# Optimization experiments

Measured on AMD Instinct MI355X. Metric: run time of the kernel, lower is better.

The kernel has to match this reference:

```python
import jax, jax.numpy as jnp
import numpy as np

N_NODES = 50000


def setup_inputs() -> dict:
    key = jax.random.key(0)
    ks = jax.random.split(key, 6)
    d_in, d_out = 256, 256
    n_edges = 1_600_000
    x = jax.random.normal(ks[0], (N_NODES, d_in), dtype=jnp.float32)
    edge_index = jax.random.randint(ks[1], (2, n_edges), 0, N_NODES, dtype=jnp.int64)
    edge_attr = jax.random.normal(ks[2], (n_edges, 16), dtype=jnp.float32)  # unused by forward
    W1 = jax.random.normal(ks[3], (d_in, d_out), dtype=jnp.float32) * (1.0 / np.sqrt(d_in))
    b1 = jnp.zeros((d_out,), dtype=jnp.float32)
    W2 = jax.random.normal(ks[4], (d_out, d_out), dtype=jnp.float32) * (1.0 / np.sqrt(d_out))
    b2 = jnp.zeros((d_out,), dtype=jnp.float32)
    eps = jnp.zeros((1,), dtype=jnp.float32)  # train_eps=True, init 0
    return {"x": x, "edge_index": edge_index, "edge_attr": edge_attr,
            "W1": W1, "b1": b1, "W2": W2, "b2": b2, "eps": eps}


def reference(x, edge_index, edge_attr, W1, b1, W2, b2, eps):
    src, dst = edge_index[0], edge_index[1]
    # sum aggregation: agg[i] = sum_{(j->i) in E} x[j]
    agg = jax.ops.segment_sum(x[src], dst, num_segments=N_NODES)  # [N, d_in]
    h = (1.0 + eps[0]) * x + agg
    # MLP: Linear -> ReLU -> (dropout=0) -> Linear
    h = jax.nn.relu(h @ W1 + b1)
    out = h @ W2 + b2
    return out
```

## Files before the change

### kernel.cpp

```cpp
#include <hip/hip_runtime.h>
#include <stdint.h>

#define NODES 50000
#define D 256
#define MP 50048
#define NBUCK 196
#define CAP 10240
#define EPB 4096
#define HS_LD 264
#define CAST_BLOCKS 12500

typedef short bf16x8 __attribute__((ext_vector_type(8)));
typedef float f32x4 __attribute__((ext_vector_type(4)));

__device__ inline unsigned short f2b(float f) {
    unsigned int u = __float_as_uint(f);
    unsigned int r = (u + 0x7fffu + ((u >> 16) & 1u)) >> 16;
    return (unsigned short)r;
}

__device__ inline bool ei_is64(const int* ei) {
    return (ei[1] | ei[3] | ei[5] | ei[7]) == 0;
}
__device__ inline int ei_get(const int* __restrict__ ei, long long pos, bool is64) {
    return is64 ? ei[2 * pos] : ei[(int)pos];
}

__global__ __launch_bounds__(256) void prep_kernel(const float* __restrict__ x,
                                                   unsigned short* __restrict__ xb,
                                                   int* __restrict__ bcnt,
                                                   const float* __restrict__ W1,
                                                   const float* __restrict__ W2,
                                                   unsigned short* __restrict__ P1,
                                                   unsigned short* __restrict__ P2,
                                                   int* __restrict__ offs, int E) {
    int blk = blockIdx.x;
    if (blk < CAST_BLOCKS) {
        if (blk == 0 && threadIdx.x < NBUCK) bcnt[threadIdx.x] = 0;
        if (blk == 0 && threadIdx.x == 0) offs[NODES] = E;
        int t = blk * 256 + threadIdx.x;
        float4 v = ((const float4*)x)[t];
        unsigned int lo = (unsigned int)f2b(v.x) | ((unsigned int)f2b(v.y) << 16);
        unsigned int hi = (unsigned int)f2b(v.z) | ((unsigned int)f2b(v.w) << 16);
        ((uint2*)xb)[t] = make_uint2(lo, hi);
    } else {
        int t = (blk - CAST_BLOCKS) * 256 + threadIdx.x;
        const float* W = (t < 8192) ? W1 : W2;
        unsigned short* P = (t < 8192) ? P1 : P2;
        int u = t & 8191;
        int lane = u & 63, nt = (u >> 6) & 15, s = u >> 10;
        int q = lane >> 4, n = nt * 16 + (lane & 15);
        int kbase = s * 32 + q * 8;
#pragma unroll
        for (int j = 0; j < 8; j++) P[u * 8 + j] = f2b(W[(kbase + j) * D + n]);
    }
}

__global__ __launch_bounds__(256) void partA_kernel(const int* __restrict__ ei, int E,
                                                    int* __restrict__ bcnt,
                                                    unsigned int* __restrict__ ebufT) {
    __shared__ int cnt[256];
    __shared__ int gbase[256];
    __shared__ int lcur[256];
    bool is64 = ei_is64(ei);
    int tid = threadIdx.x;
    cnt[tid] = 0;
    lcur[tid] = 0;
    __syncthreads();
    long long pairBase = ((long long)blockIdx.x * EPB) >> 1;
    unsigned int w[16];
    int bk[16];
#pragma unroll
    for (int r = 0; r < 8; r++) {
        long long pp = pairBase + (long long)r * 256 + tid;
        long long e0 = pp * 2;
        int s0 = 0, s1 = 0, d0 = 0, d1 = 0;
        bool v1 = (e0 + 1 < E), v0 = (e0 < E);
        if (v1) {
            if (is64) {
                uint4 sv = *(const uint4*)(ei + 4 * pp);
                uint4 dv = *(const uint4*)(ei + (size_t)2 * E + 4 * pp);
                s0 = (int)sv.x; s1 = (int)sv.z; d0 = (int)dv.x; d1 = (int)dv.z;
            } else {
                uint2 sv = *(const uint2*)(ei + 2 * pp);
                uint2 dv = *(const uint2*)(ei + (size_t)E + 2 * pp);
                s0 = (int)sv.x; s1 = (int)sv.y; d0 = (int)dv.x; d1 = (int)dv.y;
            }
        } else if (v0) {
            s0 = ei_get(ei, e0, is64);
            d0 = ei_get(ei, (long long)E + e0, is64);
        }
        bk[2 * r] = v0 ? (d0 >> 8) : -1;
        bk[2 * r + 1] = v1 ? (d1 >> 8) : -1;
        w[2 * r] = ((unsigned int)(d0 & 255) << 16) | (unsigned int)s0;
        w[2 * r + 1] = ((unsigned int)(d1 & 255) << 16) | (unsigned int)s1;
        if (v0) atomicAdd(&cnt[bk[2 * r]], 1);
        if (v1) atomicAdd(&cnt[bk[2 * r + 1]], 1);
    }
    __syncthreads();
    if (tid < NBUCK && cnt[tid] > 0) gbase[tid] = atomicAdd(&bcnt[tid], cnt[tid]);
    __syncthreads();
#pragma unroll
    for (int r = 0; r < 16; r++) {
        if (bk[r] >= 0) {
            int p = atomicAdd(&lcur[bk[r]], 1);
            ebufT[(size_t)bk[r] * CAP + gbase[bk[r]] + p] = w[r];
        }
    }
}

__global__ __launch_bounds__(1024) void partB_kernel(const int* __restrict__ bcnt,
                                                     const unsigned int* __restrict__ ebufT,
                                                     int* __restrict__ offs,
                                                     int* __restrict__ ebuf) {
    __shared__ int sb[256];
    __shared__ int ncnt[256];
    __shared__ int ncur[256];
    int b = blockIdx.x, tid = threadIdx.x;
    if (tid < 256) {
        sb[tid] = (tid < NBUCK) ? bcnt[tid] : 0;
        ncnt[tid] = 0;
    }
    __syncthreads();
    for (int off = 1; off < 256; off <<= 1) {
        int xv = 0;
        if (tid < 256 && tid >= off) xv = sb[tid - off];
        __syncthreads();
        if (tid < 256) sb[tid] += xv;
        __syncthreads();
    }
    int n = bcnt[b];
    int base = sb[b] - n;
    const unsigned int* reg = ebufT + (size_t)b * CAP;
    for (int i = tid; i < n; i += 1024) atomicAdd(&ncnt[reg[i] >> 16], 1);
    __syncthreads();
    int v = 0;
    if (tid < 256) {
        v = ncnt[tid];
        ncur[tid] = v;
    }
    __syncthreads();
    for (int off = 1; off < 256; off <<= 1) {
        int xv = 0;
        if (tid < 256 && tid >= off) xv = ncur[tid - off];
        __syncthreads();
        if (tid < 256) ncur[tid] += xv;
        __syncthreads();
    }
    if (tid < 256) {
        int excl = ncur[tid] - v;
        int node = b * 256 + tid;
        if (node < NODES) offs[node] = base + excl;
        ncur[tid] = excl;
    }
    __syncthreads();
    for (int i = tid; i < n; i += 1024) {
        unsigned int w = reg[i];
        int p = atomicAdd(&ncur[w >> 16], 1);
        ebuf[base + p] = (int)(w & 0xffffu);
    }
}

__device__ inline void upk_add(uint4 w, float* a) {
    a[0] += __uint_as_float(w.x << 16);
    a[1] += __uint_as_float(w.x & 0xffff0000u);
    a[2] += __uint_as_float(w.y << 16);
    a[3] += __uint_as_float(w.y & 0xffff0000u);
    a[4] += __uint_as_float(w.z << 16);
    a[5] += __uint_as_float(w.z & 0xffff0000u);
    a[6] += __uint_as_float(w.w << 16);
    a[7] += __uint_as_float(w.w & 0xffff0000u);
}

__global__ __launch_bounds__(256) void agg_kernel(const unsigned short* __restrict__ xb,
                                                  const int* __restrict__ offs,
                                                  const int* __restrict__ ebuf,
                                                  const float* __restrict__ eps,
                                                  unsigned short* __restrict__ h0, int colOff) {
    int wv = (blockIdx.x * 256 + threadIdx.x) >> 6;
    int lane = threadIdx.x & 63;
    if (wv >= NODES) return;
    int g = lane >> 4, l16 = lane & 15;
    const unsigned short* colBase = xb + colOff + l16 * 8;
    float aA[8] = {0, 0, 0, 0, 0, 0, 0, 0};
    float aB[8] = {0, 0, 0, 0, 0, 0, 0, 0};
    int beg = offs[wv], end = offs[wv + 1];
    int j = beg;
    for (; j + 8 <= end; j += 8) {
        int i0 = ebuf[j + g];
        int i1 = ebuf[j + 4 + g];
        uint4 w0 = *(const uint4*)(colBase + (size_t)i0 * D);
        uint4 w1 = *(const uint4*)(colBase + (size_t)i1 * D);
        upk_add(w0, aA);
        upk_add(w1, aB);
    }
    for (; j + 4 <= end; j += 4) {
        int i0 = ebuf[j + g];
        uint4 w0 = *(const uint4*)(colBase + (size_t)i0 * D);
        upk_add(w0, aA);
    }
    if (j + g < end) {
        int i0 = ebuf[j + g];
        uint4 w0 = *(const uint4*)(colBase + (size_t)i0 * D);
        upk_add(w0, aA);
    }
    float a[8];
#pragma unroll
    for (int i = 0; i < 8; i++) {
        a[i] = aA[i] + aB[i];
        a[i] += __shfl_xor(a[i], 16);
        a[i] += __shfl_xor(a[i], 32);
    }
    if (g == 0) {
        float scale = 1.0f + eps[0];
        uint4 v = *(const uint4*)(xb + (size_t)wv * D + colOff + l16 * 8);
        a[0] += scale * __uint_as_float(v.x << 16);
        a[1] += scale * __uint_as_float(v.x & 0xffff0000u);
        a[2] += scale * __uint_as_float(v.y << 16);
        a[3] += scale * __uint_as_float(v.y & 0xffff0000u);
        a[4] += scale * __uint_as_float(v.z << 16);
        a[5] += scale * __uint_as_float(v.z & 0xffff0000u);
        a[6] += scale * __uint_as_float(v.w << 16);
        a[7] += scale * __uint_as_float(v.w & 0xffff0000u);
        uint4 o;
        o.x = (unsigned int)f2b(a[0]) | ((unsigned int)f2b(a[1]) << 16);
        o.y = (unsigned int)f2b(a[2]) | ((unsigned int)f2b(a[3]) << 16);
        o.z = (unsigned int)f2b(a[4]) | ((unsigned int)f2b(a[5]) << 16);
        o.w = (unsigned int)f2b(a[6]) | ((unsigned int)f2b(a[7]) << 16);
        ((uint4*)(h0 + (size_t)wv * D + colOff))[l16] = o;
    }
}

__global__ __launch_bounds__(256) void gemm_fused_kernel(const unsigned short* __restrict__ A,
                                                         const unsigned short* __restrict__ P1,
                                                         const float* __restrict__ b1,
                                                         const unsigned short* __restrict__ P2,
                                                         const float* __restrict__ b2,
                                                         float* __restrict__ out, int Mvalid) {
    __shared__ unsigned short hs[64 * HS_LD];
    int wv = threadIdx.x >> 6;
    int lane = threadIdx.x & 63;
    int quad = lane >> 4, l16 = lane & 15;
    int mBase = blockIdx.x * 64;
    const bf16x8* B1v = (const bf16x8*)P1;
    const bf16x8* B2v = (const bf16x8*)P2;

    {
        f32x4 acc[4][4] = {};
#pragma unroll
        for (int ks = 0; ks < 8; ks++) {
            bf16x8 af[4], bf[4];
#pragma unroll
            for (int mi = 0; mi < 4; mi++) {
                int row = mBase + mi * 16 + l16;
                af[mi] = *(const bf16x8*)(A + (size_t)row * D + ks * 32 + quad * 8);
            }
#pragma unroll
            for (int ni = 0; ni < 4; ni++) bf[ni] = B1v[(ks * 16 + wv * 4 + ni) * 64 + lane];
#pragma unroll
            for (int mi = 0; mi < 4; mi++)
#pragma unroll
                for (int ni = 0; ni < 4; ni++)
                    acc[mi][ni] = __builtin_amdgcn_mfma_f32_16x16x32_bf16(af[mi], bf[ni],
                                                                          acc[mi][ni], 0, 0, 0);
        }
#pragma unroll
        for (int mi = 0; mi < 4; mi++)
#pragma unroll
            for (int ni = 0; ni < 4; ni++) {
                int col = wv * 64 + ni * 16 + l16;
                float bs = b1[col];
#pragma unroll
                for (int r = 0; r < 4; r++) {
                    int rl = mi * 16 + quad * 4 + r;
                    hs[rl * HS_LD + col] = f2b(fmaxf(acc[mi][ni][r] + bs, 0.0f));
                }
            }
    }
    __syncthreads();

    f32x4 acc[4][4] = {};
#pragma unroll
    for (int ks = 0; ks < 8; ks++) {
        bf16x8 af[4], bf[4];
#pragma unroll
        for (int mi = 0; mi < 4; mi++)
            af[mi] = *(const bf16x8*)(hs + (mi * 16 + l16) * HS_LD + ks * 32 + quad * 8);
#pragma unroll
        for (int ni = 0; ni < 4; ni++) bf[ni] = B2v[(ks * 16 + wv * 4 + ni) * 64 + lane];
#pragma unroll
        for (int mi = 0; mi < 4; mi++)
#pragma unroll
            for (int ni = 0; ni < 4; ni++)
                acc[mi][ni] =
                    __builtin_amdgcn_mfma_f32_16x16x32_bf16(af[mi], bf[ni], acc[mi][ni], 0, 0, 0);
    }
#pragma unroll
    for (int mi = 0; mi < 4; mi++)
#pragma unroll
        for (int ni = 0; ni < 4; ni++) {
            int col = wv * 64 + ni * 16 + l16;
            float bs = b2[col];
#pragma unroll
            for (int r = 0; r < 4; r++) {
                int row = mBase + mi * 16 + quad * 4 + r;
                if (row < Mvalid) out[(size_t)row * D + col] = acc[mi][ni][r] + bs;
            }
        }
}

extern "C" void kernel_launch(void* const* d_in, const int* in_sizes, int n_in,
                              void* d_out, int out_size, void* d_ws, size_t ws_size,
                              hipStream_t stream) {
    const float* x = (const float*)d_in[0];
    const int* ei = (const int*)d_in[1];
    const float* W1 = (const float*)d_in[3];
    const float* b1 = (const float*)d_in[4];
    const float* W2 = (const float*)d_in[5];
    const float* b2 = (const float*)d_in[6];
    const float* eps = (const float*)d_in[7];
    int E = in_sizes[1] / 2;

    char* p = (char*)d_ws;
    auto alloc = [&](size_t bytes) {
        char* r = p;
        p += (bytes + 255) & ~(size_t)255;
        return r;
    };
    unsigned short* xb = (unsigned short*)alloc((size_t)MP * D * 2);
    unsigned short* h0 = (unsigned short*)alloc((size_t)MP * D * 2);
    unsigned short* P1 = (unsigned short*)alloc(8192 * 8 * 2);
    unsigned short* P2 = (unsigned short*)alloc(8192 * 8 * 2);
    int* bcnt = (int*)alloc((size_t)NBUCK * 4);
    int* offs = (int*)alloc((size_t)(NODES + 1) * 4);
    int* ebuf = (int*)alloc((size_t)E * 4);
    unsigned int* ebufT = (unsigned int*)alloc((size_t)NBUCK * CAP * 4);

    prep_kernel<<<CAST_BLOCKS + 64, 256, 0, stream>>>(x, xb, bcnt, W1, W2, P1, P2, offs, E);
    partA_kernel<<<(E + EPB - 1) / EPB, 256, 0, stream>>>(ei, E, bcnt, ebufT);
    partB_kernel<<<NBUCK, 1024, 0, stream>>>(bcnt, ebufT, offs, ebuf);
    agg_kernel<<<(NODES + 3) / 4, 256, 0, stream>>>(xb, offs, ebuf, eps, h0, 0);
    agg_kernel<<<(NODES + 3) / 4, 256, 0, stream>>>(xb, offs, ebuf, eps, h0, 128);
    gemm_fused_kernel<<<MP / 64, 256, 0, stream>>>(h0, P1, b1, P2, b2, (float*)d_out, NODES);
}
```

Measured before the change: 359.3 us.

## Fuse neighbor aggregation into the MLP GEMM kernel and sort edges by source

Removes the two column-split aggregation kernels and the h0 intermediate buffer. Each GEMM block now gathers and sums the neighbor rows for its own 64 nodes straight into shared memory, one wave per row with 4 columns per lane, before running both matmuls. partB also sub-sorts each node's edge list into 8 source-index ranges so that gathers touch nearby rows, which should improve cache locality. In exchange, gather parallelism drops to 782 blocks with 16 sequential rows per wave, and each lane issues narrower 8-byte loads, so latency hiding may be weaker than in the old dedicated aggregation kernels.

```diff
diff --git a/kernel.cpp b/kernel.cpp
--- a/kernel.cpp
+++ b/kernel.cpp
@@ -114,13 +114,12 @@
                                                      int* __restrict__ offs,
                                                      int* __restrict__ ebuf) {
     __shared__ int sb[256];
-    __shared__ int ncnt[256];
-    __shared__ int ncur[256];
+    __shared__ int ncnt[2048];
+    __shared__ int ncur[2048];
+    __shared__ int nexcl[256];
     int b = blockIdx.x, tid = threadIdx.x;
-    if (tid < 256) {
-        sb[tid] = (tid < NBUCK) ? bcnt[tid] : 0;
-        ncnt[tid] = 0;
-    }
+    if (tid < 256) sb[tid] = (tid < NBUCK) ? bcnt[tid] : 0;
+    for (int i = tid; i < 2048; i += 1024) ncnt[i] = 0;
     __syncthreads();
     for (int off = 1; off < 256; off <<= 1) {
         int xv = 0;
@@ -132,116 +131,108 @@
     int n = bcnt[b];
     int base = sb[b] - n;
     const unsigned int* reg = ebufT + (size_t)b * CAP;
-    for (int i = tid; i < n; i += 1024) atomicAdd(&ncnt[reg[i] >> 16], 1);
-    __syncthreads();
-    int v = 0;
+    for (int i = tid; i < n; i += 1024) {
+        unsigned int w = reg[i];
+        atomicAdd(&ncnt[((w >> 16) << 3) | ((w & 0xffffu) >> 13)], 1);
+    }
+    __syncthreads();
     if (tid < 256) {
-        v = ncnt[tid];
-        ncur[tid] = v;
+        int s = 0;
+#pragma unroll
+        for (int c = 0; c < 8; c++) s += ncnt[tid * 8 + c];
+        nexcl[tid] = s;
     }
     __syncthreads();
     for (int off = 1; off < 256; off <<= 1) {
         int xv = 0;
-        if (tid < 256 && tid >= off) xv = ncur[tid - off];
-        __syncthreads();
-        if (tid < 256) ncur[tid] += xv;
+        if (tid < 256 && tid >= off) xv = nexcl[tid - off];
+        __syncthreads();
+        if (tid < 256) nexcl[tid] += xv;
         __syncthreads();
     }
     if (tid < 256) {
-        int excl = ncur[tid] - v;
+        int s = 0;
+#pragma unroll
+        for (int c = 0; c < 8; c++) s += ncnt[tid * 8 + c];
+        int excl = nexcl[tid] - s;
         int node = b * 256 + tid;
         if (node < NODES) offs[node] = base + excl;
-        ncur[tid] = excl;
+        int run = excl;
+#pragma unroll
+        for (int c = 0; c < 8; c++) {
+            ncur[tid * 8 + c] = run;
+            run += ncnt[tid * 8 + c];
+        }
     }
     __syncthreads();
     for (int i = tid; i < n; i += 1024) {
         unsigned int w = reg[i];
-        int p = atomicAdd(&ncur[w >> 16], 1);
+        int p = atomicAdd(&ncur[((w >> 16) << 3) | ((w & 0xffffu) >> 13)], 1);
         ebuf[base + p] = (int)(w & 0xffffu);
     }
 }
 
-__device__ inline void upk_add(uint4 w, float* a) {
+__device__ inline void upk2(uint2 w, float* a) {
     a[0] += __uint_as_float(w.x << 16);
     a[1] += __uint_as_float(w.x & 0xffff0000u);
     a[2] += __uint_as_float(w.y << 16);
     a[3] += __uint_as_float(w.y & 0xffff0000u);
-    a[4] += __uint_as_float(w.z << 16);
-    a[5] += __uint_as_float(w.z & 0xffff0000u);
-    a[6] += __uint_as_float(w.w << 16);
-    a[7] += __uint_as_float(w.w & 0xffff0000u);
-}
-
-__global__ __launch_bounds__(256) void agg_kernel(const unsigned short* __restrict__ xb,
-                                                  const int* __restrict__ offs,
-                                                  const int* __restrict__ ebuf,
-                                                  const float* __restrict__ eps,
-                                                  unsigned short* __restrict__ h0, int colOff) {
-    int wv = (blockIdx.x * 256 + threadIdx.x) >> 6;
-    int lane = threadIdx.x & 63;
-    if (wv >= NODES) return;
-    int g = lane >> 4, l16 = lane & 15;
-    const unsigned short* colBase = xb + colOff + l16 * 8;
-    float aA[8] = {0, 0, 0, 0, 0, 0, 0, 0};
-    float aB[8] = {0, 0, 0, 0, 0, 0, 0, 0};
-    int beg = offs[wv], end = offs[wv + 1];
-    int j = beg;
-    for (; j + 8 <= end; j += 8) {
-        int i0 = ebuf[j + g];
-        int i1 = ebuf[j + 4 + g];
-        uint4 w0 = *(const uint4*)(colBase + (size_t)i0 * D);
-        uint4 w1 = *(const uint4*)(colBase + (size_t)i1 * D);
-        upk_add(w0, aA);
-        upk_add(w1, aB);
-    }
-    for (; j + 4 <= end; j += 4) {
-        int i0 = ebuf[j + g];
-        uint4 w0 = *(const uint4*)(colBase + (size_t)i0 * D);
-        upk_add(w0, aA);
-    }
-    if (j + g < end) {
-        int i0 = ebuf[j + g];
-        uint4 w0 = *(const uint4*)(colBase + (size_t)i0 * D);
-        upk_add(w0, aA);
-    }
-    float a[8];
-#pragma unroll
-    for (int i = 0; i < 8; i++) {
-        a[i] = aA[i] + aB[i];
-        a[i] += __shfl_xor(a[i], 16);
-        a[i] += __shfl_xor(a[i], 32);
-    }
-    if (g == 0) {
-        float scale = 1.0f + eps[0];
-        uint4 v = *(const uint4*)(xb + (size_t)wv * D + colOff + l16 * 8);
-        a[0] += scale * __uint_as_float(v.x << 16);
-        a[1] += scale * __uint_as_float(v.x & 0xffff0000u);
-        a[2] += scale * __uint_as_float(v.y << 16);
-        a[3] += scale * __uint_as_float(v.y & 0xffff0000u);
-        a[4] += scale * __uint_as_float(v.z << 16);
-        a[5] += scale * __uint_as_float(v.z & 0xffff0000u);
-        a[6] += scale * __uint_as_float(v.w << 16);
-        a[7] += scale * __uint_as_float(v.w & 0xffff0000u);
-        uint4 o;
-        o.x = (unsigned int)f2b(a[0]) | ((unsigned int)f2b(a[1]) << 16);
-        o.y = (unsigned int)f2b(a[2]) | ((unsigned int)f2b(a[3]) << 16);
-        o.z = (unsigned int)f2b(a[4]) | ((unsigned int)f2b(a[5]) << 16);
-        o.w = (unsigned int)f2b(a[6]) | ((unsigned int)f2b(a[7]) << 16);
-        ((uint4*)(h0 + (size_t)wv * D + colOff))[l16] = o;
-    }
-}
-
-__global__ __launch_bounds__(256) void gemm_fused_kernel(const unsigned short* __restrict__ A,
-                                                         const unsigned short* __restrict__ P1,
-                                                         const float* __restrict__ b1,
-                                                         const unsigned short* __restrict__ P2,
-                                                         const float* __restrict__ b2,
-                                                         float* __restrict__ out, int Mvalid) {
+}
+
+__global__ __launch_bounds__(256) void fused_kernel(const unsigned short* __restrict__ xb,
+                                                    const int* __restrict__ offs,
+                                                    const int* __restrict__ ebuf,
+                                                    const float* __restrict__ eps,
+                                                    const unsigned short* __restrict__ P1,
+                                                    const float* __restrict__ b1,
+                                                    const unsigned short* __restrict__ P2,
+                                                    const float* __restrict__ b2,
+                                                    float* __restrict__ out, int Mvalid) {
     __shared__ unsigned short hs[64 * HS_LD];
     int wv = threadIdx.x >> 6;
     int lane = threadIdx.x & 63;
     int quad = lane >> 4, l16 = lane & 15;
     int mBase = blockIdx.x * 64;
+    float scale = 1.0f + eps[0];
+    const unsigned short* colBase = xb + lane * 4;
+
+    for (int t = 0; t < 16; ++t) {
+        int row = (wv << 4) + t;
+        int node = mBase + row;
+        float aa[4] = {0, 0, 0, 0}, bb[4] = {0, 0, 0, 0};
+        if (node < NODES) {
+            int beg = offs[node], end = offs[node + 1];
+            int j = beg;
+            for (; j + 8 <= end; j += 8) {
+                int idx[8];
+                uint2 g[8];
+#pragma unroll
+                for (int k = 0; k < 8; k++) idx[k] = ebuf[j + k];
+#pragma unroll
+                for (int k = 0; k < 8; k++)
+                    g[k] = *(const uint2*)(colBase + (size_t)idx[k] * D);
+#pragma unroll
+                for (int k = 0; k < 8; k += 2) {
+                    upk2(g[k], aa);
+                    upk2(g[k + 1], bb);
+                }
+            }
+            for (; j < end; ++j) {
+                uint2 g = *(const uint2*)(colBase + (size_t)ebuf[j] * D);
+                upk2(g, aa);
+            }
+            uint2 v = *(const uint2*)(colBase + (size_t)node * D);
+            aa[0] += scale * __uint_as_float(v.x << 16);
+            aa[1] += scale * __uint_as_float(v.x & 0xffff0000u);
+            aa[2] += scale * __uint_as_float(v.y << 16);
+            aa[3] += scale * __uint_as_float(v.y & 0xffff0000u);
+        }
+        unsigned int lo = (unsigned int)f2b(aa[0] + bb[0]) | ((unsigned int)f2b(aa[1] + bb[1]) << 16);
+        unsigned int hi = (unsigned int)f2b(aa[2] + bb[2]) | ((unsigned int)f2b(aa[3] + bb[3]) << 16);
+        *(uint2*)(hs + row * HS_LD + lane * 4) = make_uint2(lo, hi);
+    }
+    __syncthreads();
+
     const bf16x8* B1v = (const bf16x8*)P1;
     const bf16x8* B2v = (const bf16x8*)P2;
 
@@ -251,10 +242,8 @@
         for (int ks = 0; ks < 8; ks++) {
             bf16x8 af[4], bf[4];
 #pragma unroll
-            for (int mi = 0; mi < 4; mi++) {
-                int row = mBase + mi * 16 + l16;
-                af[mi] = *(const bf16x8*)(A + (size_t)row * D + ks * 32 + quad * 8);
-            }
+            for (int mi = 0; mi < 4; mi++)
+                af[mi] = *(const bf16x8*)(hs + (mi * 16 + l16) * HS_LD + ks * 32 + quad * 8);
 #pragma unroll
             for (int ni = 0; ni < 4; ni++) bf[ni] = B1v[(ks * 16 + wv * 4 + ni) * 64 + lane];
 #pragma unroll
@@ -264,6 +253,7 @@
                     acc[mi][ni] = __builtin_amdgcn_mfma_f32_16x16x32_bf16(af[mi], bf[ni],
                                                                           acc[mi][ni], 0, 0, 0);
         }
+        __syncthreads();
 #pragma unroll
         for (int mi = 0; mi < 4; mi++)
 #pragma unroll
@@ -328,7 +318,6 @@
         return r;
     };
     unsigned short* xb = (unsigned short*)alloc((size_t)MP * D * 2);
-    unsigned short* h0 = (unsigned short*)alloc((size_t)MP * D * 2);
     unsigned short* P1 = (unsigned short*)alloc(8192 * 8 * 2);
     unsigned short* P2 = (unsigned short*)alloc(8192 * 8 * 2);
     int* bcnt = (int*)alloc((size_t)NBUCK * 4);
@@ -339,7 +328,6 @@
     prep_kernel<<<CAST_BLOCKS + 64, 256, 0, stream>>>(x, xb, bcnt, W1, W2, P1, P2, offs, E);
     partA_kernel<<<(E + EPB - 1) / EPB, 256, 0, stream>>>(ei, E, bcnt, ebufT);
     partB_kernel<<<NBUCK, 1024, 0, stream>>>(bcnt, ebufT, offs, ebuf);
-    agg_kernel<<<(NODES + 3) / 4, 256, 0, stream>>>(xb, offs, ebuf, eps, h0, 0);
-    agg_kernel<<<(NODES + 3) / 4, 256, 0, stream>>>(xb, offs, ebuf, eps, h0, 128);
-    gemm_fused_kernel<<<MP / 64, 256, 0, stream>>>(h0, P1, b1, P2, b2, (float*)d_out, NODES);
-}
+    fused_kernel<<<MP / 64, 256, 0, stream>>>(xb, offs, ebuf, eps, P1, b1, P2, b2,
+                                              (float*)d_out, NODES);
+}
```

Measured after the change: 434.3 us. 20.9% more time.
